# Performance work log

Measured on AMD Instinct MI355X. Metric: run time of the kernel, lower is better.

The kernel has to match this reference:

```python
import jax, jax.numpy as jnp
import numpy as np

DIM = 1024
N_HEADS = 16
HEAD_DIM = DIM // N_HEADS


def setup_inputs() -> dict:
    key = jax.random.key(0)
    ks = jax.random.split(key, 6)
    s = DIM ** -0.5
    return {
        "x": jax.random.normal(ks[0], (2, 2048, DIM), dtype=jnp.float32),
        "Wq": jax.random.normal(ks[1], (DIM, DIM), dtype=jnp.float32) * s,
        "Wk": jax.random.normal(ks[2], (DIM, DIM), dtype=jnp.float32) * s,
        "Wv": jax.random.normal(ks[3], (DIM, DIM), dtype=jnp.float32) * s,
        "Wo": jax.random.normal(ks[4], (DIM, DIM), dtype=jnp.float32) * s,
        "bo": jax.random.normal(ks[5], (DIM,), dtype=jnp.float32) * 0.01,
    }


def reference(x, Wq, Wk, Wv, Wo, bo):
    B, T, C = x.shape
    H, D = N_HEADS, HEAD_DIM
    # Linear(dim, dim, bias=False): y = x @ W^T
    q = (x @ Wq.T).reshape(B, T, H, D).transpose(0, 2, 1, 3)  # B H T D
    k = (x @ Wk.T).reshape(B, T, H, D).transpose(0, 2, 1, 3)
    v = (x @ Wv.T).reshape(B, T, H, D).transpose(0, 2, 1, 3)
    q = q * (D ** -0.5)
    attn = jnp.einsum('bhqd,bhkd->bhqk', q, k)  # B H T T
    causal_mask = jnp.triu(jnp.ones((T, T), dtype=bool), k=1)
    attn = jnp.where(causal_mask, -jnp.inf, attn)
    attn = jax.nn.softmax(attn, axis=-1)
    out = jnp.einsum('bhqk,bhkd->bhqd', attn, v)  # B H T D
    out = out.transpose(0, 2, 1, 3).reshape(B, T, C)
    return out @ Wo.T + bo
```

## Files before the change

kernel.cpp:

```cpp
#include <hip/hip_runtime.h>
#include <math.h>

typedef __attribute__((ext_vector_type(8))) short bf16x8;
typedef __attribute__((ext_vector_type(4))) float f32x4;

__device__ __forceinline__ ushort f2bf(float f) {
  union { float f; unsigned u; } v; v.f = f;
  return (ushort)((v.u + 0x8000u) >> 16);
}

__device__ __forceinline__ void g2l16(const void* g, void* l) {
  __builtin_amdgcn_global_load_lds((const __attribute__((address_space(1))) unsigned*)g,
                                   (__attribute__((address_space(3))) unsigned*)l, 16, 0, 0);
}

__global__ __launch_bounds__(256) void cast_all(const float* __restrict__ x,
                                                const float* __restrict__ Wq,
                                                const float* __restrict__ Wk,
                                                const float* __restrict__ Wv,
                                                const float* __restrict__ Wo,
                                                ushort* __restrict__ xbf,
                                                ushort* __restrict__ wcat,
                                                float4* __restrict__ O32) {
  int i = blockIdx.x * 256 + threadIdx.x;
  if (i < 1048576) {
    float4 v = ((const float4*)x)[i];
    ushort4 u; u.x = f2bf(v.x); u.y = f2bf(v.y); u.z = f2bf(v.z); u.w = f2bf(v.w);
    ((ushort4*)xbf)[i] = u;
  } else if (i < 2097152) {
    int j = i - 1048576;
    int sel = j >> 18;
    const float* src = (sel == 0) ? Wq : (sel == 1) ? Wk : (sel == 2) ? Wv : Wo;
    float scale = (sel == 0) ? 0.125f * 1.44269504088896f : 1.0f;
    float4 v = ((const float4*)src)[j & 0x3FFFF];
    ushort4 u;
    u.x = f2bf(v.x * scale); u.y = f2bf(v.y * scale);
    u.z = f2bf(v.z * scale); u.w = f2bf(v.w * scale);
    ((ushort4*)wcat)[j] = u;
  } else {
    O32[i - 2097152] = float4{0.f, 0.f, 0.f, 0.f};
  }
}

__global__ __launch_bounds__(256) void gemm_qkv(const ushort* __restrict__ A,
                                                const ushort* __restrict__ B,
                                                ushort* __restrict__ C3) {
  const int K = 1024;
  __shared__ __align__(16) ushort As[2][128 * 32];
  __shared__ __align__(16) ushort Bs[2][128 * 32];
  const int m0 = blockIdx.y * 128, n0 = blockIdx.x * 128;
  const int tid = threadIdx.x, lane = tid & 63, wid = tid >> 6;
  const int quad = lane >> 4, lc = lane & 15;
  const int lrow = lane >> 2, lcol = (lane & 3) * 8;
  const int wm = (wid >> 1) * 64, wn = (wid & 1) * 64;

  f32x4 acc[4][4] = {};

  auto stage = [&](int k0, int nb) {
    const ushort* Ag = A + (size_t)(m0 + wid * 32 + lrow) * K + k0 + lcol;
    g2l16(Ag, &As[nb][wid * 1024]);
    g2l16(Ag + (size_t)16 * K, &As[nb][wid * 1024 + 512]);
    const ushort* Bg = B + (size_t)(n0 + wid * 32 + lrow) * K + k0 + lcol;
    g2l16(Bg, &Bs[nb][wid * 1024]);
    g2l16(Bg + (size_t)16 * K, &Bs[nb][wid * 1024 + 512]);
  };

  stage(0, 0);
  for (int k0 = 0; k0 < K; k0 += 32) {
    const int nb = (k0 >> 5) & 1;
    __syncthreads();
    if (k0 + 32 < K) stage(k0 + 32, nb ^ 1);

    bf16x8 af[4], bfr[4];
#pragma unroll
    for (int t = 0; t < 4; t++)
      af[t] = *(const bf16x8*)&As[nb][(wm + t * 16 + lc) * 32 + quad * 8];
#pragma unroll
    for (int t = 0; t < 4; t++)
      bfr[t] = *(const bf16x8*)&Bs[nb][(wn + t * 16 + lc) * 32 + quad * 8];
#pragma unroll
    for (int mt = 0; mt < 4; mt++)
#pragma unroll
      for (int nt = 0; nt < 4; nt++)
        acc[mt][nt] = __builtin_amdgcn_mfma_f32_16x16x32_bf16(af[mt], bfr[nt], acc[mt][nt], 0, 0, 0);
  }

#pragma unroll
  for (int mt = 0; mt < 4; mt++) {
#pragma unroll
    for (int r = 0; r < 4; r++) {
      int row = m0 + wm + mt * 16 + quad * 4 + r;
#pragma unroll
      for (int nt = 0; nt < 4; nt++) {
        int col = n0 + wn + nt * 16 + lc;
        size_t dst = ((size_t)(col >> 10) << 22) + (size_t)row * 1024 + (col & 1023);
        C3[dst] = f2bf(acc[mt][nt][r]);
      }
    }
  }
}

__global__ __launch_bounds__(256) void gemm_proj(const ushort* __restrict__ A,
                                                 const ushort* __restrict__ B,
                                                 float* __restrict__ C,
                                                 const float* __restrict__ bias) {
  const int K = 1024;
  __shared__ __align__(16) ushort As[2][2][128 * 32];
  __shared__ __align__(16) ushort Bs[2][2][64 * 32];
  const int m0 = blockIdx.y * 128, n0 = blockIdx.x * 64;
  const int tid = threadIdx.x, lane = tid & 63, wid = tid >> 6;
  const int quad = lane >> 4, lc = lane & 15;
  const int lrow = lane >> 2, lcol = (lane & 3) * 8;
  const int wm = (wid >> 1) * 64, wn = (wid & 1) * 32;

  f32x4 acc[4][2] = {};

  auto stage = [&](int k0, int nb) {
    const ushort* Ag = A + (size_t)(m0 + wid * 32 + lrow) * K + k0 + lcol;
    g2l16(Ag,                       &As[nb][0][wid * 1024]);
    g2l16(Ag + (size_t)16 * K,      &As[nb][0][wid * 1024 + 512]);
    g2l16(Ag + 32,                  &As[nb][1][wid * 1024]);
    g2l16(Ag + (size_t)16 * K + 32, &As[nb][1][wid * 1024 + 512]);
    const ushort* Bg = B + (size_t)(n0 + wid * 16 + lrow) * K + k0 + lcol;
    g2l16(Bg,      &Bs[nb][0][wid * 512]);
    g2l16(Bg + 32, &Bs[nb][1][wid * 512]);
  };

  stage(0, 0);
  for (int k0 = 0; k0 < K; k0 += 64) {
    const int nb = (k0 >> 6) & 1;
    __syncthreads();
    if (k0 + 64 < K) stage(k0 + 64, nb ^ 1);

#pragma unroll
    for (int ks = 0; ks < 2; ks++) {
      bf16x8 af[4], bfr[2];
#pragma unroll
      for (int t = 0; t < 4; t++)
        af[t] = *(const bf16x8*)&As[nb][ks][(wm + t * 16 + lc) * 32 + quad * 8];
#pragma unroll
      for (int t = 0; t < 2; t++)
        bfr[t] = *(const bf16x8*)&Bs[nb][ks][(wn + t * 16 + lc) * 32 + quad * 8];
#pragma unroll
      for (int mt = 0; mt < 4; mt++)
#pragma unroll
        for (int nt = 0; nt < 2; nt++)
          acc[mt][nt] = __builtin_amdgcn_mfma_f32_16x16x32_bf16(af[mt], bfr[nt], acc[mt][nt], 0, 0, 0);
    }
  }

#pragma unroll
  for (int mt = 0; mt < 4; mt++) {
#pragma unroll
    for (int r = 0; r < 4; r++) {
      int row = m0 + wm + mt * 16 + quad * 4 + r;
#pragma unroll
      for (int nt = 0; nt < 2; nt++) {
        int col = n0 + wn + nt * 16 + lc;
        C[(size_t)row * 1024 + col] = acc[mt][nt][r] + bias[col];
      }
    }
  }
}

__global__ __launch_bounds__(256) void transpose_v(const ushort* __restrict__ Vb,
                                                   ushort* __restrict__ Vt) {
  __shared__ ushort tile[64][72];
  const int bh = blockIdx.y, b = bh >> 4, h = bh & 15;
  const int tt = blockIdx.x;
  const int tid = threadIdx.x;
#pragma unroll
  for (int i = 0; i < 2; i++) {
    int idx = i * 256 + tid;
    int trow = idx >> 3;
    int dcol = (idx & 7) * 8;
    uint4 v = *(const uint4*)(Vb + (size_t)(b * 2048 + tt * 64 + trow) * 1024 + h * 64 + dcol);
    ushort e[8]; *(uint4*)e = v;
#pragma unroll
    for (int j = 0; j < 8; j++) tile[dcol + j][trow] = e[j];
  }
  __syncthreads();
#pragma unroll
  for (int i = 0; i < 2; i++) {
    int idx = i * 256 + tid;
    int drow = idx >> 3;
    int tloc = (idx & 7) * 8;
    uint4 v = *(const uint4*)&tile[drow][tloc];
    *(uint4*)(Vt + (size_t)bh * 131072 + (size_t)drow * 2048 + tt * 64 + tloc) = v;
  }
}

__global__ __launch_bounds__(256, 4) void attn_kernel(const ushort* __restrict__ Qb,
                                                      const ushort* __restrict__ Kb,
                                                      const ushort* __restrict__ Vt,
                                                      float* __restrict__ O32,
                                                      float* __restrict__ L32) {
  __shared__ __align__(16) ushort Ks[2][64 * 32];
  __shared__ __align__(16) ushort Vs[2][64 * 32];
  __shared__ __align__(16) ushort Ps[4][32][72];

  const int bh = blockIdx.y, b = bh >> 4, h = bh & 15;
  const int f = (int)blockIdx.x;
  int qi, ci;
  if (f < 16)      { qi = 12 + (f >> 2); ci = f & 3; }
  else if (f < 28) { int g = f - 16; int q3 = g / 3; qi = 8 + q3; ci = g - 3 * q3; }
  else if (f < 36) { int g = f - 28; qi = 4 + (g >> 1); ci = g & 1; }
  else             { qi = f - 36; ci = 0; }
  const int t0 = ci * 8;
  const int t1 = min(t0 + 8, 2 * qi + 2);

  const int tid = threadIdx.x, lane = tid & 63, wid = tid >> 6;
  const int quad = lane >> 4, lc = lane & 15;
  const int lrow = lane >> 2, lcol = (lane & 3) * 8;
  const int qbw = qi * 128 + wid * 32;

  const size_t kbase = (size_t)(b * 2048) * 1024 + h * 64;
  const size_t vbase = (size_t)bh * 131072;

  bf16x8 qf[2][2];
#pragma unroll
  for (int t = 0; t < 2; t++) {
    const ushort* Qp = Qb + kbase + (size_t)(qbw + t * 16 + lc) * 1024;
    qf[t][0] = *(const bf16x8*)(Qp + quad * 8);
    qf[t][1] = *(const bf16x8*)(Qp + 32 + quad * 8);
  }

  f32x4 o_acc[2][4] = {};
  float l_r[2][4] = {};

  for (int kt = t0; kt < t1; kt++) {
    const int kb = kt * 64;
    __syncthreads();
#pragma unroll
    for (int cc = 0; cc < 2; cc++) {
      int ck = wid + cc * 4;
      int half = ck >> 2, rg = ck & 3;
      const ushort* gK = Kb + kbase + (size_t)(kb + rg * 16 + lrow) * 1024 + half * 32 + lcol;
      g2l16(gK, &Ks[half][rg * 512]);
      const ushort* gV = Vt + vbase + (size_t)(rg * 16 + lrow) * 2048 + kb + half * 32 + lcol;
      g2l16(gV, &Vs[half][rg * 512]);
    }
    __syncthreads();

#pragma unroll
    for (int c = 0; c < 4; c++) {
      bf16x8 kf0 = *(const bf16x8*)&Ks[0][(c * 16 + lc) * 32 + quad * 8];
      bf16x8 kf1 = *(const bf16x8*)&Ks[1][(c * 16 + lc) * 32 + quad * 8];
#pragma unroll
      for (int t = 0; t < 2; t++) {
        f32x4 z = {};
        z = __builtin_amdgcn_mfma_f32_16x16x32_bf16(qf[t][0], kf0, z, 0, 0, 0);
        z = __builtin_amdgcn_mfma_f32_16x16x32_bf16(qf[t][1], kf1, z, 0, 0, 0);
        const bool diag = (kb + 63 > qbw + t * 16);
#pragma unroll
        for (int r = 0; r < 4; r++) {
          float sv = z[r];
          if (diag && (kb + c * 16 + lc > qbw + t * 16 + quad * 4 + r)) sv = -1e30f;
          float pv = __builtin_amdgcn_exp2f(sv);
          l_r[t][r] += pv;
          Ps[wid][t * 16 + quad * 4 + r][c * 16 + lc] = f2bf(pv);
        }
      }
    }
    __asm__ volatile("s_waitcnt lgkmcnt(0)" ::: "memory");
    bf16x8 ap[2][2];
#pragma unroll
    for (int t = 0; t < 2; t++) {
      ap[t][0] = *(const bf16x8*)&Ps[wid][t * 16 + lc][quad * 8];
      ap[t][1] = *(const bf16x8*)&Ps[wid][t * 16 + lc][32 + quad * 8];
    }

#pragma unroll
    for (int nt = 0; nt < 4; nt++) {
      bf16x8 vb0 = *(const bf16x8*)&Vs[0][(nt * 16 + lc) * 32 + quad * 8];
      bf16x8 vb1 = *(const bf16x8*)&Vs[1][(nt * 16 + lc) * 32 + quad * 8];
#pragma unroll
      for (int t = 0; t < 2; t++) {
        o_acc[t][nt] = __builtin_amdgcn_mfma_f32_16x16x32_bf16(ap[t][0], vb0, o_acc[t][nt], 0, 0, 0);
        o_acc[t][nt] = __builtin_amdgcn_mfma_f32_16x16x32_bf16(ap[t][1], vb1, o_acc[t][nt], 0, 0, 0);
      }
    }
  }

#pragma unroll
  for (int t = 0; t < 2; t++) {
#pragma unroll
    for (int r = 0; r < 4; r++) {
      float s_ = l_r[t][r];
      s_ += __shfl_xor(s_, 1);
      s_ += __shfl_xor(s_, 2);
      s_ += __shfl_xor(s_, 4);
      s_ += __shfl_xor(s_, 8);
      l_r[t][r] = s_;
    }
    if (lc == 0) {
#pragma unroll
      for (int r = 0; r < 4; r++)
        atomicAdd(&L32[(size_t)bh * 2048 + qbw + t * 16 + quad * 4 + r], l_r[t][r]);
    }
#pragma unroll
    for (int r = 0; r < 4; r++) {
      size_t orow = ((size_t)(b * 2048) + qbw + t * 16 + quad * 4 + r) * 1024 + h * 64 + lc;
#pragma unroll
      for (int nt = 0; nt < 4; nt++)
        atomicAdd(&O32[orow + nt * 16], o_acc[t][nt][r]);
    }
  }
}

__global__ __launch_bounds__(256) void normalize_kernel(const float* __restrict__ O32,
                                                        const float* __restrict__ L32,
                                                        ushort* __restrict__ Out) {
  const int row = blockIdx.x;
  const int tid = threadIdx.x;
  const int col = tid * 4;
  const int b = row >> 11, t = row & 2047, h = col >> 6;
  const float inv = 1.0f / L32[(size_t)(b * 16 + h) * 2048 + t];
  float4 o = ((const float4*)(O32 + (size_t)row * 1024))[tid];
  ushort4 u;
  u.x = f2bf(o.x * inv); u.y = f2bf(o.y * inv);
  u.z = f2bf(o.z * inv); u.w = f2bf(o.w * inv);
  ((ushort4*)(Out + (size_t)row * 1024))[tid] = u;
}

extern "C" void kernel_launch(void* const* d_in, const int* in_sizes, int n_in,
                              void* d_out, int out_size, void* d_ws, size_t ws_size,
                              hipStream_t stream) {
  const float* x  = (const float*)d_in[0];
  const float* Wq = (const float*)d_in[1];
  const float* Wk = (const float*)d_in[2];
  const float* Wv = (const float*)d_in[3];
  const float* Wo = (const float*)d_in[4];
  const float* bo = (const float*)d_in[5];
  float* out = (float*)d_out;

  char* ws = (char*)d_ws;
  ushort* xbf  = (ushort*)(ws);
  ushort* wcat = (ushort*)(ws + (8ull  << 20));
  ushort* qkv  = (ushort*)(ws + (16ull << 20));
  ushort* Qp   = qkv;
  ushort* Kp   = qkv + (1ull << 22);
  ushort* Vp   = qkv + (2ull << 22);
  ushort* Vt   = (ushort*)(ws);
  float*  L32  = (float*)Vp;
  float*  O32  = out;
  ushort* attn_out = Qp;

  cast_all<<<12288, 256, 0, stream>>>(x, Wq, Wk, Wv, Wo, xbf, wcat, (float4*)O32);

  gemm_qkv<<<dim3(24, 32), 256, 0, stream>>>(xbf, wcat, qkv);

  transpose_v<<<dim3(32, 32), 256, 0, stream>>>(Vp, Vt);

  hipMemsetAsync(L32, 0, (size_t)32 * 2048 * 4, stream);

  attn_kernel<<<dim3(40, 32), 256, 0, stream>>>(Qp, Kp, Vt, O32, L32);

  normalize_kernel<<<4096, 256, 0, stream>>>(O32, L32, attn_out);

  gemm_proj<<<dim3(16, 32), 256, 0, stream>>>(
      attn_out, wcat + (size_t)3072 * 1024, out, bo);
}
```

Before: 212.5 us.

## Halve attention block size, compute row sums via MFMA, fold L32 zeroing into transpose

```diff
diff --git a/kernel.cpp b/kernel.cpp
--- a/kernel.cpp
+++ b/kernel.cpp
@@ -164,11 +164,17 @@
 }
 
 __global__ __launch_bounds__(256) void transpose_v(const ushort* __restrict__ Vb,
-                                                   ushort* __restrict__ Vt) {
+                                                   ushort* __restrict__ Vt,
+                                                   float4* __restrict__ L32z) {
   __shared__ ushort tile[64][72];
   const int bh = blockIdx.y, b = bh >> 4, h = bh & 15;
   const int tt = blockIdx.x;
   const int tid = threadIdx.x;
+  if (bh == 0) {
+    int base = (tt * 256 + tid) * 2;
+    L32z[base]     = float4{0.f, 0.f, 0.f, 0.f};
+    L32z[base + 1] = float4{0.f, 0.f, 0.f, 0.f};
+  }
 #pragma unroll
   for (int i = 0; i < 2; i++) {
     int idx = i * 256 + tid;
@@ -190,29 +196,29 @@
   }
 }
 
-__global__ __launch_bounds__(256, 4) void attn_kernel(const ushort* __restrict__ Qb,
+__global__ __launch_bounds__(128, 3) void attn_kernel(const ushort* __restrict__ Qb,
                                                       const ushort* __restrict__ Kb,
                                                       const ushort* __restrict__ Vt,
                                                       float* __restrict__ O32,
                                                       float* __restrict__ L32) {
   __shared__ __align__(16) ushort Ks[2][64 * 32];
   __shared__ __align__(16) ushort Vs[2][64 * 32];
-  __shared__ __align__(16) ushort Ps[4][32][72];
+  __shared__ __align__(16) ushort Ps[2][32][72];
 
   const int bh = blockIdx.y, b = bh >> 4, h = bh & 15;
-  const int f = (int)blockIdx.x;
+  const int f = 79 - (int)blockIdx.x;
   int qi, ci;
-  if (f < 16)      { qi = 12 + (f >> 2); ci = f & 3; }
-  else if (f < 28) { int g = f - 16; int q3 = g / 3; qi = 8 + q3; ci = g - 3 * q3; }
-  else if (f < 36) { int g = f - 28; qi = 4 + (g >> 1); ci = g & 1; }
-  else             { qi = f - 36; ci = 0; }
+  if (f < 8)       { qi = f;                 ci = 0; }
+  else if (f < 24) { int g = f - 8;  qi = 8  + (g >> 1); ci = g & 1; }
+  else if (f < 48) { int g = f - 24; int q3 = g / 3; qi = 16 + q3; ci = g - 3 * q3; }
+  else             { int g = f - 48; qi = 24 + (g >> 2); ci = g & 3; }
   const int t0 = ci * 8;
-  const int t1 = min(t0 + 8, 2 * qi + 2);
+  const int t1 = min(t0 + 8, qi + 1);
 
   const int tid = threadIdx.x, lane = tid & 63, wid = tid >> 6;
   const int quad = lane >> 4, lc = lane & 15;
   const int lrow = lane >> 2, lcol = (lane & 3) * 8;
-  const int qbw = qi * 128 + wid * 32;
+  const int qbw = qi * 64 + wid * 32;
 
   const size_t kbase = (size_t)(b * 2048) * 1024 + h * 64;
   const size_t vbase = (size_t)bh * 131072;
@@ -225,40 +231,45 @@
     qf[t][1] = *(const bf16x8*)(Qp + 32 + quad * 8);
   }
 
+  bf16x8 ones;
+#pragma unroll
+  for (int j = 0; j < 8; j++) ones[j] = (short)0x3f80;
+
   f32x4 o_acc[2][4] = {};
-  float l_r[2][4] = {};
+  f32x4 l_acc[2] = {};
 
   for (int kt = t0; kt < t1; kt++) {
     const int kb = kt * 64;
     __syncthreads();
 #pragma unroll
-    for (int cc = 0; cc < 2; cc++) {
-      int ck = wid + cc * 4;
-      int half = ck >> 2, rg = ck & 3;
-      const ushort* gK = Kb + kbase + (size_t)(kb + rg * 16 + lrow) * 1024 + half * 32 + lcol;
-      g2l16(gK, &Ks[half][rg * 512]);
-      const ushort* gV = Vt + vbase + (size_t)(rg * 16 + lrow) * 2048 + kb + half * 32 + lcol;
-      g2l16(gV, &Vs[half][rg * 512]);
+    for (int j = 0; j < 4; j++) {
+      const ushort* gK = Kb + kbase + (size_t)(kb + j * 16 + lrow) * 1024 + wid * 32 + lcol;
+      g2l16(gK, &Ks[wid][j * 512]);
+      const ushort* gV = Vt + vbase + (size_t)(j * 16 + lrow) * 2048 + kb + wid * 32 + lcol;
+      g2l16(gV, &Vs[wid][j * 512]);
     }
     __syncthreads();
 
+    bf16x8 kf[4][2];
 #pragma unroll
     for (int c = 0; c < 4; c++) {
-      bf16x8 kf0 = *(const bf16x8*)&Ks[0][(c * 16 + lc) * 32 + quad * 8];
-      bf16x8 kf1 = *(const bf16x8*)&Ks[1][(c * 16 + lc) * 32 + quad * 8];
+      kf[c][0] = *(const bf16x8*)&Ks[0][(c * 16 + lc) * 32 + quad * 8];
+      kf[c][1] = *(const bf16x8*)&Ks[1][(c * 16 + lc) * 32 + quad * 8];
+    }
+
+#pragma unroll
+    for (int c = 0; c < 4; c++) {
 #pragma unroll
       for (int t = 0; t < 2; t++) {
         f32x4 z = {};
-        z = __builtin_amdgcn_mfma_f32_16x16x32_bf16(qf[t][0], kf0, z, 0, 0, 0);
-        z = __builtin_amdgcn_mfma_f32_16x16x32_bf16(qf[t][1], kf1, z, 0, 0, 0);
+        z = __builtin_amdgcn_mfma_f32_16x16x32_bf16(qf[t][0], kf[c][0], z, 0, 0, 0);
+        z = __builtin_amdgcn_mfma_f32_16x16x32_bf16(qf[t][1], kf[c][1], z, 0, 0, 0);
         const bool diag = (kb + 63 > qbw + t * 16);
 #pragma unroll
         for (int r = 0; r < 4; r++) {
           float sv = z[r];
           if (diag && (kb + c * 16 + lc > qbw + t * 16 + quad * 4 + r)) sv = -1e30f;
-          float pv = __builtin_amdgcn_exp2f(sv);
-          l_r[t][r] += pv;
-          Ps[wid][t * 16 + quad * 4 + r][c * 16 + lc] = f2bf(pv);
+          Ps[wid][t * 16 + quad * 4 + r][c * 16 + lc] = f2bf(__builtin_amdgcn_exp2f(sv));
         }
       }
     }
@@ -268,6 +279,12 @@
     for (int t = 0; t < 2; t++) {
       ap[t][0] = *(const bf16x8*)&Ps[wid][t * 16 + lc][quad * 8];
       ap[t][1] = *(const bf16x8*)&Ps[wid][t * 16 + lc][32 + quad * 8];
+    }
+
+#pragma unroll
+    for (int t = 0; t < 2; t++) {
+      l_acc[t] = __builtin_amdgcn_mfma_f32_16x16x32_bf16(ap[t][0], ones, l_acc[t], 0, 0, 0);
+      l_acc[t] = __builtin_amdgcn_mfma_f32_16x16x32_bf16(ap[t][1], ones, l_acc[t], 0, 0, 0);
     }
 
 #pragma unroll
@@ -284,19 +301,10 @@
 
 #pragma unroll
   for (int t = 0; t < 2; t++) {
-#pragma unroll
-    for (int r = 0; r < 4; r++) {
-      float s_ = l_r[t][r];
-      s_ += __shfl_xor(s_, 1);
-      s_ += __shfl_xor(s_, 2);
-      s_ += __shfl_xor(s_, 4);
-      s_ += __shfl_xor(s_, 8);
-      l_r[t][r] = s_;
-    }
     if (lc == 0) {
 #pragma unroll
       for (int r = 0; r < 4; r++)
-        atomicAdd(&L32[(size_t)bh * 2048 + qbw + t * 16 + quad * 4 + r], l_r[t][r]);
+        atomicAdd(&L32[(size_t)bh * 2048 + qbw + t * 16 + quad * 4 + r], l_acc[t][r]);
     }
 #pragma unroll
     for (int r = 0; r < 4; r++) {
@@ -342,7 +350,7 @@
   ushort* Kp   = qkv + (1ull << 22);
   ushort* Vp   = qkv + (2ull << 22);
   ushort* Vt   = (ushort*)(ws);
-  float*  L32  = (float*)Vp;
+  float*  L32  = (float*)(ws + (12ull << 20));
   float*  O32  = out;
   ushort* attn_out = Qp;
 
@@ -350,11 +358,9 @@
 
   gemm_qkv<<<dim3(24, 32), 256, 0, stream>>>(xbf, wcat, qkv);
 
-  transpose_v<<<dim3(32, 32), 256, 0, stream>>>(Vp, Vt);
-
-  hipMemsetAsync(L32, 0, (size_t)32 * 2048 * 4, stream);
-
-  attn_kernel<<<dim3(40, 32), 256, 0, stream>>>(Qp, Kp, Vt, O32, L32);
+  transpose_v<<<dim3(32, 32), 256, 0, stream>>>(Vp, Vt, (float4*)L32);
+
+  attn_kernel<<<dim3(80, 32), 128, 0, stream>>>(Qp, Kp, Vt, O32, L32);
 
   normalize_kernel<<<4096, 256, 0, stream>>>(O32, L32, attn_out);
 
```

Result: faster. 206.2 us (-3.0%).
